# Optimization experiments

Hardware: AMD Instinct MI355X
Metric: run time of the kernel (lower is better)

The kernel has to match this reference:

```python
import jax, jax.numpy as jnp
import numpy as np

N_FEAT = 256
N_HID = 128
N_HEAD = 4
N_HEAD_LAST = 6
N_CLASS = 40
NEG_SLOPE = 0.2


def gat_conv(x, src, dst, W, att_src, att_dst, bias, heads, ch, concat):
    # x: [N, in], W: [in, heads*ch], att_*: [heads, ch]
    N = x.shape[0]
    xw = (x @ W).reshape(N, heads, ch)                      # [N, H, C]
    a_src = jnp.sum(xw * att_src, axis=-1)                  # [N, H]
    a_dst = jnp.sum(xw * att_dst, axis=-1)                  # [N, H]
    e = jax.nn.leaky_relu(a_src[src] + a_dst[dst], NEG_SLOPE)  # [E, H]
    # softmax over incoming edges of each destination node
    m = jax.ops.segment_max(e, dst, num_segments=N)         # [N, H]
    ex = jnp.exp(e - m[dst])
    denom = jax.ops.segment_sum(ex, dst, num_segments=N)    # [N, H]
    alpha = ex / (denom[dst] + 1e-16)                       # [E, H]
    msg = xw[src] * alpha[..., None]                        # [E, H, C]
    out = jax.ops.segment_sum(msg, dst, num_segments=N)     # [N, H, C]
    out = out.reshape(N, heads * ch) if concat else out.mean(axis=1)
    return out + bias


def setup_inputs() -> dict:
    key = jax.random.key(0)
    ks = jax.random.split(key, 16)
    N, E = 10000, 160000
    x = jax.random.normal(ks[0], (N, N_FEAT), dtype=jnp.float32)
    edge_index = jax.random.randint(ks[1], (2, E), 0, N, dtype=jnp.int64)
    hid = N_HID * N_HEAD  # 512
    s = lambda fan: 1.0 / np.sqrt(fan)
    return {
        "x": x,
        "edge_index": edge_index,
        "W0": jax.random.normal(ks[2], (N_FEAT, hid), jnp.float32) * s(N_FEAT),
        "a_src0": jax.random.normal(ks[3], (N_HEAD, N_HID), jnp.float32) * s(N_HID),
        "a_dst0": jax.random.normal(ks[4], (N_HEAD, N_HID), jnp.float32) * s(N_HID),
        "b0": jnp.zeros((hid,), jnp.float32),
        "Wskip_in": jax.random.normal(ks[5], (N_FEAT, hid), jnp.float32) * s(N_FEAT),
        "W1": jax.random.normal(ks[6], (hid, hid), jnp.float32) * s(hid),
        "a_src1": jax.random.normal(ks[7], (N_HEAD, N_HID), jnp.float32) * s(N_HID),
        "a_dst1": jax.random.normal(ks[8], (N_HEAD, N_HID), jnp.float32) * s(N_HID),
        "b1": jnp.zeros((hid,), jnp.float32),
        "W2": jax.random.normal(ks[9], (hid, N_HEAD_LAST * N_CLASS), jnp.float32) * s(hid),
        "a_src2": jax.random.normal(ks[10], (N_HEAD_LAST, N_CLASS), jnp.float32) * s(N_CLASS),
        "a_dst2": jax.random.normal(ks[11], (N_HEAD_LAST, N_CLASS), jnp.float32) * s(N_CLASS),
        "b2": jnp.zeros((N_CLASS,), jnp.float32),
        "Wskip_out": jax.random.normal(ks[12], (hid, N_CLASS), jnp.float32) * s(hid),
    }


def reference(x, edge_index, W0, a_src0, a_dst0, b0, Wskip_in,
              W1, a_src1, a_dst1, b1,
              W2, a_src2, a_dst2, b2, Wskip_out):
    N = x.shape[0]
    loops = jnp.arange(N, dtype=edge_index.dtype)
    src = jnp.concatenate([edge_index[0], loops])  # add self loops (PyG GATConv)
    dst = jnp.concatenate([edge_index[1], loops])
    # eval mode: dropout is identity
    h = gat_conv(x, src, dst, W0, a_src0, a_dst0, b0, N_HEAD, N_HID, True)
    x1 = jax.nn.elu(h + x @ Wskip_in)                      # res skip w/ projection
    h = gat_conv(x1, src, dst, W1, a_src1, a_dst1, b1, N_HEAD, N_HID, True)
    x2 = jax.nn.elu(h + x1)                                # res skip, same dims
    h = gat_conv(x2, src, dst, W2, a_src2, a_dst2, b2, N_HEAD_LAST, N_CLASS, False)
    out = h + x2 @ Wskip_out                               # out_skip 'res'
    return out
```

## Files before the change

kernel.cpp:

```cpp
#include <hip/hip_runtime.h>
#include <math.h>


#define N_FEAT 256
#define HID 512

using u16 = unsigned short;
using bf16x8 = __attribute__((ext_vector_type(8))) __bf16;
using f32x16 = __attribute__((ext_vector_type(16))) float;

__device__ inline u16 bf16_rne(float f) {
    unsigned u = __float_as_uint(f);
    return (u16)((u + 0x7fffu + ((u >> 16) & 1u)) >> 16);
}
__device__ inline float bf16_to_f32(u16 h) {
    return __uint_as_float((unsigned)h << 16);
}
__device__ inline bf16x8 ldb8(const u16* p) {
    return *reinterpret_cast<const bf16x8*>(p);
}


__global__ void init_counts(int* cursor, int N) {
    int i = blockIdx.x * blockDim.x + threadIdx.x;
    if (i < N) cursor[i] = 1;
}

__global__ void count_edges(const int* __restrict__ ei, int E, int* cursor) {
    int e = blockIdx.x * blockDim.x + threadIdx.x;
    if (e < E) atomicAdd(&cursor[ei[E + e]], 1);
}

__global__ __launch_bounds__(1024) void scan_offsets(int* cursor, int* row_off, int N) {
    __shared__ int sdata[1024];
    int tid = threadIdx.x;
    int chunk = (N + 1023) >> 10;
    int base = tid * chunk;
    int lsum = 0;
    for (int i = 0; i < chunk; i++) {
        int idx = base + i;
        if (idx < N) lsum += cursor[idx];
    }
    sdata[tid] = lsum;
    __syncthreads();
    for (int off = 1; off < 1024; off <<= 1) {
        int t = (tid >= off) ? sdata[tid - off] : 0;
        __syncthreads();
        sdata[tid] += t;
        __syncthreads();
    }
    int run = sdata[tid] - lsum;
    if (tid == 0) row_off[0] = 0;
    for (int i = 0; i < chunk; i++) {
        int idx = base + i;
        if (idx < N) {
            int c = cursor[idx];
            cursor[idx] = run;
            run += c;
            row_off[idx + 1] = run;
        }
    }
}

__global__ void fill_csr(const int* __restrict__ ei, int E, int N,
                         int* cursor, int* __restrict__ col) {
    int i = blockIdx.x * blockDim.x + threadIdx.x;
    int tot = E + N;
    if (i >= tot) return;
    int s, d;
    if (i < E) { s = ei[i]; d = ei[E + i]; }
    else       { s = i - E; d = s; }
    int pos = atomicAdd(&cursor[d], 1);
    col[pos] = s;
}


__global__ __launch_bounds__(256) void att_combine(const float* __restrict__ W,
                                                   const float* __restrict__ as_,
                                                   const float* __restrict__ ad_,
                                                   float* __restrict__ ac,
                                                   int K, int H, int C) {
    int i = blockIdx.x * blockDim.x + threadIdx.x;
    if (i >= K * 2 * H) return;
    int k = i / (2 * H);
    int hh = i - k * 2 * H;
    int h = (hh >= H) ? hh - H : hh;
    const float* av = (hh >= H) ? &ad_[h * C] : &as_[h * C];
    const float* wp = &W[(size_t)k * H * C + (size_t)h * C];
    float sum = 0.f;
    for (int c = 0; c < C; c++) sum = fmaf(wp[c], av[c], sum);
    ac[(size_t)k * 2 * H + hh] = sum;
}


__global__ __launch_bounds__(256) void cvtA_pack(const float* __restrict__ X,
                                                 u16* __restrict__ hi, u16* __restrict__ lo,
                                                 int M, int K, int Rblocks) {
    int gid = blockIdx.x * blockDim.x + threadIdx.x;
    int lane = gid & 63;
    int rest = gid >> 6;
    int KC = K >> 4;
    int R = rest / KC;
    int c = rest - R * KC;
    if (R >= Rblocks) return;
    int row = R * 32 + (lane & 31);
    if (row >= M) row = M - 1;
    const float* src = X + (size_t)row * K + c * 16 + (lane >> 5) * 8;
    float4 v0 = *reinterpret_cast<const float4*>(src);
    float4 v1 = *reinterpret_cast<const float4*>(src + 4);
    float vv[8] = {v0.x, v0.y, v0.z, v0.w, v1.x, v1.y, v1.z, v1.w};
    unsigned hp[4], lp[4];
    #pragma unroll
    for (int j = 0; j < 4; j++) {
        u16 h0 = bf16_rne(vv[2 * j]);
        u16 h1 = bf16_rne(vv[2 * j + 1]);
        float r0 = vv[2 * j]     - __uint_as_float((unsigned)h0 << 16);
        float r1 = vv[2 * j + 1] - __uint_as_float((unsigned)h1 << 16);
        u16 l0 = bf16_rne(r0);
        u16 l1 = bf16_rne(r1);
        hp[j] = (unsigned)h0 | ((unsigned)h1 << 16);
        lp[j] = (unsigned)l0 | ((unsigned)l1 << 16);
    }
    size_t dst = ((size_t)rest * 64 + lane) * 8;
    *reinterpret_cast<int4*>(hi + dst) = make_int4(hp[0], hp[1], hp[2], hp[3]);
    *reinterpret_cast<int4*>(lo + dst) = make_int4(lp[0], lp[1], lp[2], lp[3]);
}

__global__ __launch_bounds__(256) void cvtB_pack(const float* __restrict__ B,
                                                 u16* __restrict__ hi, u16* __restrict__ lo,
                                                 int K, int Nb, int Cblocks) {
    int gid = blockIdx.x * blockDim.x + threadIdx.x;
    int lane = gid & 63;
    int rest = gid >> 6;
    int KC = K >> 4;
    int Cb = rest / KC;
    int c = rest - Cb * KC;
    if (Cb >= Cblocks) return;
    int n = Cb * 32 + (lane & 31);
    int kbase = c * 16 + (lane >> 5) * 8;
    float vv[8];
    #pragma unroll
    for (int j = 0; j < 8; j++)
        vv[j] = (n < Nb) ? B[(size_t)(kbase + j) * Nb + n] : 0.f;
    unsigned hp[4], lp[4];
    #pragma unroll
    for (int j = 0; j < 4; j++) {
        u16 h0 = bf16_rne(vv[2 * j]);
        u16 h1 = bf16_rne(vv[2 * j + 1]);
        float r0 = vv[2 * j]     - __uint_as_float((unsigned)h0 << 16);
        float r1 = vv[2 * j + 1] - __uint_as_float((unsigned)h1 << 16);
        u16 l0 = bf16_rne(r0);
        u16 l1 = bf16_rne(r1);
        hp[j] = (unsigned)h0 | ((unsigned)h1 << 16);
        lp[j] = (unsigned)l0 | ((unsigned)l1 << 16);
    }
    size_t dst = ((size_t)rest * 64 + lane) * 8;
    *reinterpret_cast<int4*>(hi + dst) = make_int4(hp[0], hp[1], hp[2], hp[3]);
    *reinterpret_cast<int4*>(lo + dst) = make_int4(lp[0], lp[1], lp[2], lp[3]);
}


__global__ __launch_bounds__(256) void gemm_fused(const u16* __restrict__ Ahi,
                                                  const u16* __restrict__ Alo,
                                                  const u16* __restrict__ Bhi,
                                                  const u16* __restrict__ Blo,
                                                  u16* __restrict__ xwb, int xwCols,
                                                  float* __restrict__ skipP,
                                                  int skipBeg, int skipEnd,
                                                  float* __restrict__ asrc,
                                                  float* __restrict__ adst,
                                                  int attBeg, int H,
                                                  int M, int K,
                                                  int ntiles, int Rblocks) {
    int nwg = gridDim.x, b = blockIdx.x;
    int q = nwg >> 3, r = nwg & 7;
    int xcd = b & 7, idx = b >> 3;
    int t = (xcd < r) ? (xcd * (q + 1) + idx)
                      : (r * (q + 1) + (xcd - r) * q + idx);
    int bm = (t / ntiles) * 128;
    int bn = (t - (t / ntiles) * ntiles) * 64;

    int lane = threadIdx.x & 63, w = threadIdx.x >> 6;
    int wr = w >> 1, wc = w & 1;
    int l31 = lane & 31, lg = lane >> 5;
    int KC = K >> 4;

    int R0 = (bm + wr * 64) >> 5;
    int R1 = R0 + 1;
    if (R0 >= Rblocks) R0 = Rblocks - 1;
    if (R1 >= Rblocks) R1 = Rblocks - 1;
    int Cb = (bn + wc * 32) >> 5;

    const u16* pa0h = Ahi + (((size_t)R0 * KC) * 64 + lane) * 8;
    const u16* pa0l = Alo + (((size_t)R0 * KC) * 64 + lane) * 8;
    const u16* pa1h = Ahi + (((size_t)R1 * KC) * 64 + lane) * 8;
    const u16* pa1l = Alo + (((size_t)R1 * KC) * 64 + lane) * 8;
    const u16* pbh  = Bhi + (((size_t)Cb * KC) * 64 + lane) * 8;
    const u16* pbl  = Blo + (((size_t)Cb * KC) * 64 + lane) * 8;

    f32x16 acc0, acc1;
    #pragma unroll
    for (int i2 = 0; i2 < 16; i2++) { acc0[i2] = 0.f; acc1[i2] = 0.f; }

    bf16x8 a0h = ldb8(pa0h), a0l = ldb8(pa0l);
    bf16x8 a1h = ldb8(pa1h), a1l = ldb8(pa1l);
    bf16x8 bh  = ldb8(pbh),  bl  = ldb8(pbl);

    for (int c = 1; c <= KC; c++) {
        size_t off = (size_t)c * 512;
        bf16x8 na0h = ldb8(pa0h + off), na0l = ldb8(pa0l + off);
        bf16x8 na1h = ldb8(pa1h + off), na1l = ldb8(pa1l + off);
        bf16x8 nbh  = ldb8(pbh + off),  nbl  = ldb8(pbl + off);
        acc0 = __builtin_amdgcn_mfma_f32_32x32x16_bf16(a0h, bh, acc0, 0, 0, 0);
        acc1 = __builtin_amdgcn_mfma_f32_32x32x16_bf16(a1h, bh, acc1, 0, 0, 0);
        acc0 = __builtin_amdgcn_mfma_f32_32x32x16_bf16(a0h, bl, acc0, 0, 0, 0);
        acc1 = __builtin_amdgcn_mfma_f32_32x32x16_bf16(a1h, bl, acc1, 0, 0, 0);
        acc0 = __builtin_amdgcn_mfma_f32_32x32x16_bf16(a0l, bh, acc0, 0, 0, 0);
        acc1 = __builtin_amdgcn_mfma_f32_32x32x16_bf16(a1l, bh, acc1, 0, 0, 0);
        a0h = na0h; a0l = na0l; a1h = na1h; a1l = na1l; bh = nbh; bl = nbl;
    }

    int n = bn + wc * 32 + l31;
    int base_m = bm + wr * 64;
    #pragma unroll
    for (int rg = 0; rg < 16; rg++) {
        int mrow = (rg & 3) + 8 * (rg >> 2) + 4 * lg;
        int m0 = base_m + mrow;
        int m1 = m0 + 32;
        float v0 = acc0[rg], v1 = acc1[rg];
        if (n < xwCols) {
            if (m0 < M) xwb[(size_t)m0 * xwCols + n] = bf16_rne(v0);
            if (m1 < M) xwb[(size_t)m1 * xwCols + n] = bf16_rne(v1);
        } else if (n >= skipBeg && n < skipEnd) {
            int cc = n - skipBeg, st = skipEnd - skipBeg;
            if (m0 < M) skipP[(size_t)m0 * st + cc] = v0;
            if (m1 < M) skipP[(size_t)m1 * st + cc] = v1;
        } else if (n >= attBeg && n < attBeg + H) {
            int h = n - attBeg;
            if (m0 < M) asrc[(size_t)m0 * H + h] = v0;
            if (m1 < M) asrc[(size_t)m1 * H + h] = v1;
        } else if (n >= attBeg + H && n < attBeg + 2 * H) {
            int h = n - attBeg - H;
            if (m0 < M) adst[(size_t)m0 * H + h] = v0;
            if (m1 < M) adst[(size_t)m1 * H + h] = v1;
        }
    }
}


template <int H, int CHUNKS>
__global__ __launch_bounds__(256) void edge_alpha_fused(const float* __restrict__ asrc,
                                                        const float* __restrict__ adst,
                                                        const int* __restrict__ row_off,
                                                        const int* __restrict__ col,
                                                        float* __restrict__ alpha,
                                                        int N) {
    int w = (blockIdx.x * blockDim.x + threadIdx.x) >> 6;
    int lane = threadIdx.x & 63;
    if (w >= N) return;
    int jb = row_off[w], je = row_off[w + 1];

    float adn[H];
    #pragma unroll
    for (int h = 0; h < H; h++) adn[h] = adst[(size_t)w * H + h];

    float ev[CHUNKS][H];
    float m[H];
    #pragma unroll
    for (int h = 0; h < H; h++) m[h] = -INFINITY;

    #pragma unroll
    for (int c = 0; c < CHUNKS; c++) {
        int j = jb + c * 64 + lane;
        if (j < je) {
            int s = col[j];
            const float* ap = &asrc[(size_t)s * H];
            #pragma unroll
            for (int h = 0; h < H; h++) {
                float e = ap[h] + adn[h];
                e = e > 0.f ? e : 0.2f * e;
                ev[c][h] = e;
                m[h] = fmaxf(m[h], e);
            }
        } else {
            #pragma unroll
            for (int h = 0; h < H; h++) ev[c][h] = -INFINITY;
        }
    }
    for (int j = jb + CHUNKS * 64 + lane; j < je; j += 64) {
        int s = col[j];
        const float* ap = &asrc[(size_t)s * H];
        #pragma unroll
        for (int h = 0; h < H; h++) {
            float e = ap[h] + adn[h];
            e = e > 0.f ? e : 0.2f * e;
            m[h] = fmaxf(m[h], e);
        }
    }

    #pragma unroll
    for (int off = 32; off; off >>= 1)
        #pragma unroll
        for (int h = 0; h < H; h++) m[h] = fmaxf(m[h], __shfl_xor(m[h], off));

    float ssum[H];
    #pragma unroll
    for (int h = 0; h < H; h++) ssum[h] = 0.f;
    #pragma unroll
    for (int c = 0; c < CHUNKS; c++)
        #pragma unroll
        for (int h = 0; h < H; h++) ssum[h] += __expf(ev[c][h] - m[h]);
    for (int j = jb + CHUNKS * 64 + lane; j < je; j += 64) {
        int s = col[j];
        const float* ap = &asrc[(size_t)s * H];
        #pragma unroll
        for (int h = 0; h < H; h++) {
            float e = ap[h] + adn[h];
            e = e > 0.f ? e : 0.2f * e;
            ssum[h] += __expf(e - m[h]);
        }
    }
    #pragma unroll
    for (int off = 32; off; off >>= 1)
        #pragma unroll
        for (int h = 0; h < H; h++) ssum[h] += __shfl_xor(ssum[h], off);

    float inv[H];
    #pragma unroll
    for (int h = 0; h < H; h++) inv[h] = 1.f / (ssum[h] + 1e-16f);

    #pragma unroll
    for (int c = 0; c < CHUNKS; c++) {
        int j = jb + c * 64 + lane;
        if (j < je) {
            float* op = &alpha[(size_t)j * H];
            #pragma unroll
            for (int h = 0; h < H; h++)
                op[h] = __expf(ev[c][h] - m[h]) * inv[h];
        }
    }
    for (int j = jb + CHUNKS * 64 + lane; j < je; j += 64) {
        int s = col[j];
        const float* ap = &asrc[(size_t)s * H];
        float* op = &alpha[(size_t)j * H];
        #pragma unroll
        for (int h = 0; h < H; h++) {
            float e = ap[h] + adn[h];
            e = e > 0.f ? e : 0.2f * e;
            op[h] = __expf(e - m[h]) * inv[h];
        }
    }
}


template <int SKIPPK>
__global__ __launch_bounds__(256) void agg_fused512(const u16* __restrict__ xw,
                                                    const float* __restrict__ alpha,
                                                    const int* __restrict__ row_off,
                                                    const int* __restrict__ col,
                                                    const float* __restrict__ bias,
                                                    const float* __restrict__ skipF,
                                                    const u16* __restrict__ skipHi,
                                                    const u16* __restrict__ skipLo,
                                                    u16* __restrict__ outHi,
                                                    u16* __restrict__ outLo,
                                                    int N) {
    int w = (blockIdx.x * blockDim.x + threadIdx.x) >> 6;
    int lane = threadIdx.x & 63;
    if (w >= N) return;
    int base = lane * 8;
    int hme = lane >> 4;

    float acc[8] = {};
    int jb = row_off[w], je = row_off[w + 1];

    int j = jb;
    for (; j + 3 < je; j += 4) {
        int s0 = col[j], s1 = col[j + 1], s2 = col[j + 2], s3 = col[j + 3];
        float a0 = alpha[(size_t)(j + 0) * 4 + hme];
        float a1 = alpha[(size_t)(j + 1) * 4 + hme];
        float a2 = alpha[(size_t)(j + 2) * 4 + hme];
        float a3 = alpha[(size_t)(j + 3) * 4 + hme];
        uint4 r0 = *reinterpret_cast<const uint4*>(&xw[(size_t)s0 * 512 + base]);
        uint4 r1 = *reinterpret_cast<const uint4*>(&xw[(size_t)s1 * 512 + base]);
        uint4 r2 = *reinterpret_cast<const uint4*>(&xw[(size_t)s2 * 512 + base]);
        uint4 r3 = *reinterpret_cast<const uint4*>(&xw[(size_t)s3 * 512 + base]);
        acc[0] = fmaf(a0, __uint_as_float(r0.x << 16), acc[0]);
        acc[1] = fmaf(a0, __uint_as_float(r0.x & 0xffff0000u), acc[1]);
        acc[2] = fmaf(a0, __uint_as_float(r0.y << 16), acc[2]);
        acc[3] = fmaf(a0, __uint_as_float(r0.y & 0xffff0000u), acc[3]);
        acc[4] = fmaf(a0, __uint_as_float(r0.z << 16), acc[4]);
        acc[5] = fmaf(a0, __uint_as_float(r0.z & 0xffff0000u), acc[5]);
        acc[6] = fmaf(a0, __uint_as_float(r0.w << 16), acc[6]);
        acc[7] = fmaf(a0, __uint_as_float(r0.w & 0xffff0000u), acc[7]);
        acc[0] = fmaf(a1, __uint_as_float(r1.x << 16), acc[0]);
        acc[1] = fmaf(a1, __uint_as_float(r1.x & 0xffff0000u), acc[1]);
        acc[2] = fmaf(a1, __uint_as_float(r1.y << 16), acc[2]);
        acc[3] = fmaf(a1, __uint_as_float(r1.y & 0xffff0000u), acc[3]);
        acc[4] = fmaf(a1, __uint_as_float(r1.z << 16), acc[4]);
        acc[5] = fmaf(a1, __uint_as_float(r1.z & 0xffff0000u), acc[5]);
        acc[6] = fmaf(a1, __uint_as_float(r1.w << 16), acc[6]);
        acc[7] = fmaf(a1, __uint_as_float(r1.w & 0xffff0000u), acc[7]);
        acc[0] = fmaf(a2, __uint_as_float(r2.x << 16), acc[0]);
        acc[1] = fmaf(a2, __uint_as_float(r2.x & 0xffff0000u), acc[1]);
        acc[2] = fmaf(a2, __uint_as_float(r2.y << 16), acc[2]);
        acc[3] = fmaf(a2, __uint_as_float(r2.y & 0xffff0000u), acc[3]);
        acc[4] = fmaf(a2, __uint_as_float(r2.z << 16), acc[4]);
        acc[5] = fmaf(a2, __uint_as_float(r2.z & 0xffff0000u), acc[5]);
        acc[6] = fmaf(a2, __uint_as_float(r2.w << 16), acc[6]);
        acc[7] = fmaf(a2, __uint_as_float(r2.w & 0xffff0000u), acc[7]);
        acc[0] = fmaf(a3, __uint_as_float(r3.x << 16), acc[0]);
        acc[1] = fmaf(a3, __uint_as_float(r3.x & 0xffff0000u), acc[1]);
        acc[2] = fmaf(a3, __uint_as_float(r3.y << 16), acc[2]);
        acc[3] = fmaf(a3, __uint_as_float(r3.y & 0xffff0000u), acc[3]);
        acc[4] = fmaf(a3, __uint_as_float(r3.z << 16), acc[4]);
        acc[5] = fmaf(a3, __uint_as_float(r3.z & 0xffff0000u), acc[5]);
        acc[6] = fmaf(a3, __uint_as_float(r3.w << 16), acc[6]);
        acc[7] = fmaf(a3, __uint_as_float(r3.w & 0xffff0000u), acc[7]);
    }
    for (; j < je; ++j) {
        int s = col[j];
        float a = alpha[(size_t)j * 4 + hme];
        uint4 raw = *reinterpret_cast<const uint4*>(&xw[(size_t)s * 512 + base]);
        acc[0] = fmaf(a, __uint_as_float(raw.x << 16), acc[0]);
        acc[1] = fmaf(a, __uint_as_float(raw.x & 0xffff0000u), acc[1]);
        acc[2] = fmaf(a, __uint_as_float(raw.y << 16), acc[2]);
        acc[3] = fmaf(a, __uint_as_float(raw.y & 0xffff0000u), acc[3]);
        acc[4] = fmaf(a, __uint_as_float(raw.z << 16), acc[4]);
        acc[5] = fmaf(a, __uint_as_float(raw.z & 0xffff0000u), acc[5]);
        acc[6] = fmaf(a, __uint_as_float(raw.w << 16), acc[6]);
        acc[7] = fmaf(a, __uint_as_float(raw.w & 0xffff0000u), acc[7]);
    }

    int R = w >> 5, r31 = w & 31, cc = lane >> 1, sub = lane & 1;
    int lp = r31 | (sub << 5);
    size_t slot = (((size_t)R * 32 + cc) * 64 + lp) * 8;

    float sk[8];
    if (SKIPPK) {
        int4 h4 = *reinterpret_cast<const int4*>(skipHi + slot);
        int4 l4 = *reinterpret_cast<const int4*>(skipLo + slot);
        unsigned hu[4] = {(unsigned)h4.x, (unsigned)h4.y, (unsigned)h4.z, (unsigned)h4.w};
        unsigned lu[4] = {(unsigned)l4.x, (unsigned)l4.y, (unsigned)l4.z, (unsigned)l4.w};
        #pragma unroll
        for (int i = 0; i < 4; i++) {
            sk[2 * i]     = __uint_as_float(hu[i] << 16) + __uint_as_float(lu[i] << 16);
            sk[2 * i + 1] = __uint_as_float(hu[i] & 0xffff0000u)
                          + __uint_as_float(lu[i] & 0xffff0000u);
        }
    } else {
        const float* kp = &skipF[(size_t)w * 512 + base];
        float4 s0 = *reinterpret_cast<const float4*>(kp);
        float4 s1 = *reinterpret_cast<const float4*>(kp + 4);
        sk[0] = s0.x; sk[1] = s0.y; sk[2] = s0.z; sk[3] = s0.w;
        sk[4] = s1.x; sk[5] = s1.y; sk[6] = s1.z; sk[7] = s1.w;
    }

    const float* bp = &bias[base];
    float r[8];
    #pragma unroll
    for (int i = 0; i < 8; i++) {
        float v = acc[i] + bp[i] + sk[i];
        r[i] = v > 0.f ? v : expm1f(v);
    }

    unsigned hp[4], lpk[4];
    #pragma unroll
    for (int i = 0; i < 4; i++) {
        u16 h0 = bf16_rne(r[2 * i]);
        u16 h1 = bf16_rne(r[2 * i + 1]);
        float q0 = r[2 * i]     - __uint_as_float((unsigned)h0 << 16);
        float q1 = r[2 * i + 1] - __uint_as_float((unsigned)h1 << 16);
        u16 l0 = bf16_rne(q0);
        u16 l1 = bf16_rne(q1);
        hp[i]  = (unsigned)h0 | ((unsigned)h1 << 16);
        lpk[i] = (unsigned)l0 | ((unsigned)l1 << 16);
    }
    *reinterpret_cast<int4*>(outHi + slot) = make_int4(hp[0], hp[1], hp[2], hp[3]);
    *reinterpret_cast<int4*>(outLo + slot) = make_int4(lpk[0], lpk[1], lpk[2], lpk[3]);
}


__global__ __launch_bounds__(256) void agg_final240(const u16* __restrict__ xw,
                                                    const float* __restrict__ alpha,
                                                    const int* __restrict__ row_off,
                                                    const int* __restrict__ col,
                                                    const float* __restrict__ b2,
                                                    const float* __restrict__ skip,
                                                    float* __restrict__ out,
                                                    int N) {
    int w = (blockIdx.x * blockDim.x + threadIdx.x) >> 6;
    int lane = threadIdx.x & 63;
    if (w >= N) return;
    bool active = lane < 40;

    float acc[6] = {};
    int jb = row_off[w], je = row_off[w + 1];

    int j = jb;
    for (; j + 1 < je; j += 2) {
        int s0 = col[j], s1 = col[j + 1];
        const float* ap0 = &alpha[(size_t)j * 6];
        const float* ap1 = &alpha[(size_t)(j + 1) * 6];
        if (active) {
            const u16* sp0 = &xw[(size_t)s0 * 240 + lane];
            const u16* sp1 = &xw[(size_t)s1 * 240 + lane];
            #pragma unroll
            for (int h = 0; h < 6; h++) {
                acc[h] = fmaf(ap0[h], bf16_to_f32(sp0[h * 40]), acc[h]);
                acc[h] = fmaf(ap1[h], bf16_to_f32(sp1[h * 40]), acc[h]);
            }
        }
    }
    for (; j < je; ++j) {
        int s = col[j];
        const float* ap = &alpha[(size_t)j * 6];
        if (active) {
            const u16* sp = &xw[(size_t)s * 240 + lane];
            #pragma unroll
            for (int h = 0; h < 6; h++)
                acc[h] = fmaf(ap[h], bf16_to_f32(sp[h * 40]), acc[h]);
        }
    }
    if (active) {
        float v = (acc[0] + acc[1] + acc[2] + acc[3] + acc[4] + acc[5]) * (1.f / 6.f)
                  + b2[lane] + skip[(size_t)w * 40 + lane];
        out[(size_t)w * 40 + lane] = v;
    }
}


extern "C" void kernel_launch(void* const* d_in, const int* in_sizes, int n_in,
                              void* d_out, int out_size, void* d_ws, size_t ws_size,
                              hipStream_t stream) {
    const float* x        = (const float*)d_in[0];
    const int*   ei       = (const int*)  d_in[1];
    const float* W0       = (const float*)d_in[2];
    const float* a_src0   = (const float*)d_in[3];
    const float* a_dst0   = (const float*)d_in[4];
    const float* b0       = (const float*)d_in[5];
    const float* Wskip_in = (const float*)d_in[6];
    const float* W1       = (const float*)d_in[7];
    const float* a_src1   = (const float*)d_in[8];
    const float* a_dst1   = (const float*)d_in[9];
    const float* b1       = (const float*)d_in[10];
    const float* W2       = (const float*)d_in[11];
    const float* a_src2   = (const float*)d_in[12];
    const float* a_dst2   = (const float*)d_in[13];
    const float* b2       = (const float*)d_in[14];
    const float* Wskip_out= (const float*)d_in[15];

    const int N = in_sizes[0] / N_FEAT;
    const int E = in_sizes[1] / 2;
    float* out = (float*)d_out;

    const int Rblocks = (N + 31) / 32;
    const int mtiles = (N + 127) / 128;

    float* ws = (float*)d_ws;
    size_t o = 0;
    u16* xwb   = (u16*)(ws + o); o += (size_t)N * 256;
    float* tmpD  = ws + o; o += (size_t)N * HID;
    float* asrc  = ws + o; o += (size_t)N * 8;
    float* adst  = ws + o; o += (size_t)N * 8;
    float* skipo = ws + o; o += (size_t)N * 40;
    float* alpha = ws + o; o += (size_t)(E + N) * 6;
    float* ac    = ws + o; o += (size_t)512 * 12;

    u16* up = (u16*)(ws + o);
    size_t uo = 0;
    const size_t aPack = (size_t)Rblocks * 32 * 512 + 512;
    u16* AhA = up + uo; uo += aPack;   u16* AlA = up + uo; uo += aPack;
    u16* AhB = up + uo; uo += aPack;   u16* AlB = up + uo; uo += aPack;
    const size_t b0sz = (size_t)34 * 16 * 512 + 512;
    u16* B0h = up + uo; uo += b0sz;  u16* B0l = up + uo; uo += b0sz;
    const size_t b1sz = (size_t)18 * 32 * 512 + 512;
    u16* B1h = up + uo; uo += b1sz;  u16* B1l = up + uo; uo += b1sz;
    const size_t b2sz = (size_t)12 * 32 * 512 + 512;
    u16* B2h = up + uo; uo += b2sz;  u16* B2l = up + uo; uo += b2sz;
    int* row_off = (int*)(up + uo);
    int* cursor  = row_off + (N + 1);
    int* col     = cursor + (N + 1);

    init_counts<<<(N + 255) / 256, 256, 0, stream>>>(cursor, N);
    count_edges<<<(E + 255) / 256, 256, 0, stream>>>(ei, E, cursor);
    scan_offsets<<<1, 1024, 0, stream>>>(cursor, row_off, N);
    fill_csr<<<(E + N + 255) / 256, 256, 0, stream>>>(ei, E, N, cursor, col);

    cvtB_pack<<<(16 * 16 * 64 + 255) / 256, 256, 0, stream>>>(W0, B0h, B0l, 256, 512, 16);
    cvtB_pack<<<(16 * 16 * 64 + 255) / 256, 256, 0, stream>>>(
        Wskip_in, B0h + (size_t)16 * 16 * 512, B0l + (size_t)16 * 16 * 512, 256, 512, 16);
    att_combine<<<(256 * 8 + 255) / 256, 256, 0, stream>>>(W0, a_src0, a_dst0, ac, 256, 4, 128);
    cvtB_pack<<<(2 * 16 * 64 + 255) / 256, 256, 0, stream>>>(
        ac, B0h + (size_t)32 * 16 * 512, B0l + (size_t)32 * 16 * 512, 256, 8, 2);
    cvtB_pack<<<(16 * 32 * 64 + 255) / 256, 256, 0, stream>>>(W1, B1h, B1l, 512, 512, 16);
    att_combine<<<(512 * 8 + 255) / 256, 256, 0, stream>>>(W1, a_src1, a_dst1, ac, 512, 4, 128);
    cvtB_pack<<<(2 * 32 * 64 + 255) / 256, 256, 0, stream>>>(
        ac, B1h + (size_t)16 * 32 * 512, B1l + (size_t)16 * 32 * 512, 512, 8, 2);
    cvtB_pack<<<(8 * 32 * 64 + 255) / 256, 256, 0, stream>>>(W2, B2h, B2l, 512, 240, 8);
    cvtB_pack<<<(2 * 32 * 64 + 255) / 256, 256, 0, stream>>>(
        Wskip_out, B2h + (size_t)8 * 32 * 512, B2l + (size_t)8 * 32 * 512, 512, 40, 2);
    att_combine<<<(512 * 12 + 255) / 256, 256, 0, stream>>>(W2, a_src2, a_dst2, ac, 512, 6, 40);
    cvtB_pack<<<(2 * 32 * 64 + 255) / 256, 256, 0, stream>>>(
        ac, B2h + (size_t)10 * 32 * 512, B2l + (size_t)10 * 32 * 512, 512, 12, 2);

    int nodeBlocks = (N * 64 + 255) / 256;
    const int BIG = 1 << 30;

    cvtA_pack<<<(Rblocks * 16 * 64 + 255) / 256, 256, 0, stream>>>(x, AhA, AlA, N, 256, Rblocks);
    gemm_fused<<<mtiles * 17, 256, 0, stream>>>(
        AhA, AlA, B0h, B0l, xwb, 512, tmpD, 512, 1024, asrc, adst, 1024, 4,
        N, 256, 17, Rblocks);
    edge_alpha_fused<4, 4><<<nodeBlocks, 256, 0, stream>>>(asrc, adst, row_off, col, alpha, N);
    agg_fused512<0><<<nodeBlocks, 256, 0, stream>>>(
        xwb, alpha, row_off, col, b0, tmpD, nullptr, nullptr, AhB, AlB, N);

    gemm_fused<<<mtiles * 9, 256, 0, stream>>>(
        AhB, AlB, B1h, B1l, xwb, 512, nullptr, BIG, BIG, asrc, adst, 512, 4,
        N, 512, 9, Rblocks);
    edge_alpha_fused<4, 4><<<nodeBlocks, 256, 0, stream>>>(asrc, adst, row_off, col, alpha, N);
    agg_fused512<1><<<nodeBlocks, 256, 0, stream>>>(
        xwb, alpha, row_off, col, b1, nullptr, AhB, AlB, AhA, AlA, N);

    gemm_fused<<<mtiles * 6, 256, 0, stream>>>(
        AhA, AlA, B2h, B2l, xwb, 240, skipo, 256, 296, asrc, adst, 320, 6,
        N, 512, 6, Rblocks);
    edge_alpha_fused<6, 4><<<nodeBlocks, 256, 0, stream>>>(asrc, adst, row_off, col, alpha, N);
    agg_final240<<<nodeBlocks, 256, 0, stream>>>(
        xwb, alpha, row_off, col, b2, skipo, out, N);
}
```

Measured before the change: 415.6 us.

## Fuse edge softmax into aggregation via shared memory and batch weight packing launches

The separate per-layer edge_alpha kernel is folded into the aggregation kernels. Each wave computes its node's attention softmax, keeps the source indices and alpha values in LDS, and then gathers from LDS, so the global alpha array write and re-read go away. Nodes with more than 256 edges recompute alpha on the fly for the overflow edges. Separately, the many small att_combine and cvtB_pack launches are merged into two launches. This adds LDS use (about 20KB per block) and a block barrier, which may lower occupancy.

```diff
diff --git a/kernel.cpp b/kernel.cpp
--- a/kernel.cpp
+++ b/kernel.cpp
@@ -75,18 +75,24 @@
 }
 
 
-__global__ __launch_bounds__(256) void att_combine(const float* __restrict__ W,
-                                                   const float* __restrict__ as_,
-                                                   const float* __restrict__ ad_,
-                                                   float* __restrict__ ac,
-                                                   int K, int H, int C) {
+__global__ __launch_bounds__(256) void att_combine_all(
+        const float* __restrict__ W0, const float* __restrict__ as0, const float* __restrict__ ad0,
+        const float* __restrict__ W1, const float* __restrict__ as1, const float* __restrict__ ad1,
+        const float* __restrict__ W2, const float* __restrict__ as2, const float* __restrict__ ad2,
+        float* __restrict__ ac0, float* __restrict__ ac1, float* __restrict__ ac2) {
     int i = blockIdx.x * blockDim.x + threadIdx.x;
-    if (i >= K * 2 * H) return;
-    int k = i / (2 * H);
-    int hh = i - k * 2 * H;
+    const float *W, *as_, *ad_;
+    float* ac;
+    int K, H, C, li;
+    if (i < 2048)       { W = W0; as_ = as0; ad_ = ad0; ac = ac0; K = 256; H = 4; C = 128; li = i; }
+    else if (i < 6144)  { W = W1; as_ = as1; ad_ = ad1; ac = ac1; K = 512; H = 4; C = 128; li = i - 2048; }
+    else if (i < 12288) { W = W2; as_ = as2; ad_ = ad2; ac = ac2; K = 512; H = 6; C = 40;  li = i - 6144; }
+    else return;
+    int k = li / (2 * H);
+    int hh = li - k * 2 * H;
     int h = (hh >= H) ? hh - H : hh;
-    const float* av = (hh >= H) ? &ad_[h * C] : &as_[h * C];
-    const float* wp = &W[(size_t)k * H * C + (size_t)h * C];
+    const float* av = ((hh >= H) ? ad_ : as_) + h * C;
+    const float* wp = W + (size_t)k * H * C + (size_t)h * C;
     float sum = 0.f;
     for (int c = 0; c < C; c++) sum = fmaf(wp[c], av[c], sum);
     ac[(size_t)k * 2 * H + hh] = sum;
@@ -126,16 +132,14 @@
     *reinterpret_cast<int4*>(lo + dst) = make_int4(lp[0], lp[1], lp[2], lp[3]);
 }
 
-__global__ __launch_bounds__(256) void cvtB_pack(const float* __restrict__ B,
-                                                 u16* __restrict__ hi, u16* __restrict__ lo,
-                                                 int K, int Nb, int Cblocks) {
-    int gid = blockIdx.x * blockDim.x + threadIdx.x;
+__device__ inline void cvtB_body(const float* __restrict__ B,
+                                 u16* __restrict__ hi, u16* __restrict__ lo,
+                                 int K, int Nb, int gid) {
     int lane = gid & 63;
     int rest = gid >> 6;
     int KC = K >> 4;
     int Cb = rest / KC;
     int c = rest - Cb * KC;
-    if (Cb >= Cblocks) return;
     int n = Cb * 32 + (lane & 31);
     int kbase = c * 16 + (lane >> 5) * 8;
     float vv[8];
@@ -157,6 +161,24 @@
     size_t dst = ((size_t)rest * 64 + lane) * 8;
     *reinterpret_cast<int4*>(hi + dst) = make_int4(hp[0], hp[1], hp[2], hp[3]);
     *reinterpret_cast<int4*>(lo + dst) = make_int4(lp[0], lp[1], lp[2], lp[3]);
+}
+
+__global__ __launch_bounds__(256) void pack_all_B(
+        const float* __restrict__ W0, const float* __restrict__ Wsi, const float* __restrict__ ac0,
+        const float* __restrict__ W1, const float* __restrict__ ac1,
+        const float* __restrict__ W2, const float* __restrict__ Wso, const float* __restrict__ ac2,
+        u16* __restrict__ B0h, u16* __restrict__ B0l,
+        u16* __restrict__ B1h, u16* __restrict__ B1l,
+        u16* __restrict__ B2h, u16* __restrict__ B2l) {
+    int g = blockIdx.x * blockDim.x + threadIdx.x;
+    if (g < 16384)      cvtB_body(W0,  B0h, B0l, 256, 512, g);
+    else if (g < 32768) cvtB_body(Wsi, B0h + (size_t)16 * 16 * 512, B0l + (size_t)16 * 16 * 512, 256, 512, g - 16384);
+    else if (g < 34816) cvtB_body(ac0, B0h + (size_t)32 * 16 * 512, B0l + (size_t)32 * 16 * 512, 256, 8,   g - 32768);
+    else if (g < 67584) cvtB_body(W1,  B1h, B1l, 512, 512, g - 34816);
+    else if (g < 71680) cvtB_body(ac1, B1h + (size_t)16 * 32 * 512, B1l + (size_t)16 * 32 * 512, 512, 8,   g - 67584);
+    else if (g < 88064) cvtB_body(W2,  B2h, B2l, 512, 240, g - 71680);
+    else if (g < 92160) cvtB_body(Wso, B2h + (size_t)8 * 32 * 512,  B2l + (size_t)8 * 32 * 512,  512, 40,  g - 88064);
+    else if (g < 96256) cvtB_body(ac2, B2h + (size_t)10 * 32 * 512, B2l + (size_t)10 * 32 * 512, 512, 12,  g - 92160);
 }
 
 
@@ -248,143 +270,125 @@
 }
 
 
-template <int H, int CHUNKS>
-__global__ __launch_bounds__(256) void edge_alpha_fused(const float* __restrict__ asrc,
-                                                        const float* __restrict__ adst,
-                                                        const int* __restrict__ row_off,
-                                                        const int* __restrict__ col,
-                                                        float* __restrict__ alpha,
-                                                        int N) {
+template <int SKIPPK>
+__global__ __launch_bounds__(256) void agg_sm512(const u16* __restrict__ xw,
+                                                 const float* __restrict__ asrc,
+                                                 const float* __restrict__ adst,
+                                                 const int* __restrict__ row_off,
+                                                 const int* __restrict__ col,
+                                                 const float* __restrict__ bias,
+                                                 const float* __restrict__ skipF,
+                                                 const u16* __restrict__ skipHi,
+                                                 const u16* __restrict__ skipLo,
+                                                 u16* __restrict__ outHi,
+                                                 u16* __restrict__ outLo,
+                                                 int N) {
+    __shared__ float lalpha[4][256 * 4];
+    __shared__ int   lcol[4][256];
     int w = (blockIdx.x * blockDim.x + threadIdx.x) >> 6;
     int lane = threadIdx.x & 63;
-    if (w >= N) return;
-    int jb = row_off[w], je = row_off[w + 1];
-
-    float adn[H];
-    #pragma unroll
-    for (int h = 0; h < H; h++) adn[h] = adst[(size_t)w * H + h];
-
-    float ev[CHUNKS][H];
-    float m[H];
-    #pragma unroll
-    for (int h = 0; h < H; h++) m[h] = -INFINITY;
-
-    #pragma unroll
-    for (int c = 0; c < CHUNKS; c++) {
-        int j = jb + c * 64 + lane;
-        if (j < je) {
+    int wid = (threadIdx.x >> 6) & 3;
+    bool valid = w < N;
+    int jb = 0, je = 0;
+    float adn[4], m[4], inv[4];
+
+    if (valid) {
+        jb = row_off[w]; je = row_off[w + 1];
+        float4 ad4 = *reinterpret_cast<const float4*>(&adst[(size_t)w * 4]);
+        adn[0] = ad4.x; adn[1] = ad4.y; adn[2] = ad4.z; adn[3] = ad4.w;
+
+        float ev[4][4];
+        int scol[4];
+        #pragma unroll
+        for (int h = 0; h < 4; h++) m[h] = -INFINITY;
+
+        #pragma unroll
+        for (int c = 0; c < 4; c++) {
+            int j = jb + c * 64 + lane;
+            if (j < je) {
+                int s = col[j]; scol[c] = s;
+                float4 as4 = *reinterpret_cast<const float4*>(&asrc[(size_t)s * 4]);
+                float e0 = as4.x + adn[0]; e0 = e0 > 0.f ? e0 : 0.2f * e0;
+                float e1 = as4.y + adn[1]; e1 = e1 > 0.f ? e1 : 0.2f * e1;
+                float e2 = as4.z + adn[2]; e2 = e2 > 0.f ? e2 : 0.2f * e2;
+                float e3 = as4.w + adn[3]; e3 = e3 > 0.f ? e3 : 0.2f * e3;
+                ev[c][0] = e0; ev[c][1] = e1; ev[c][2] = e2; ev[c][3] = e3;
+                m[0] = fmaxf(m[0], e0); m[1] = fmaxf(m[1], e1);
+                m[2] = fmaxf(m[2], e2); m[3] = fmaxf(m[3], e3);
+            } else {
+                scol[c] = -1;
+                #pragma unroll
+                for (int h = 0; h < 4; h++) ev[c][h] = -INFINITY;
+            }
+        }
+        for (int j = jb + 256 + lane; j < je; j += 64) {
             int s = col[j];
-            const float* ap = &asrc[(size_t)s * H];
-            #pragma unroll
-            for (int h = 0; h < H; h++) {
-                float e = ap[h] + adn[h];
+            #pragma unroll
+            for (int h = 0; h < 4; h++) {
+                float e = asrc[(size_t)s * 4 + h] + adn[h];
                 e = e > 0.f ? e : 0.2f * e;
-                ev[c][h] = e;
                 m[h] = fmaxf(m[h], e);
             }
-        } else {
-            #pragma unroll
-            for (int h = 0; h < H; h++) ev[c][h] = -INFINITY;
-        }
-    }
-    for (int j = jb + CHUNKS * 64 + lane; j < je; j += 64) {
-        int s = col[j];
-        const float* ap = &asrc[(size_t)s * H];
-        #pragma unroll
-        for (int h = 0; h < H; h++) {
-            float e = ap[h] + adn[h];
-            e = e > 0.f ? e : 0.2f * e;
-            m[h] = fmaxf(m[h], e);
-        }
-    }
-
-    #pragma unroll
-    for (int off = 32; off; off >>= 1)
-        #pragma unroll
-        for (int h = 0; h < H; h++) m[h] = fmaxf(m[h], __shfl_xor(m[h], off));
-
-    float ssum[H];
-    #pragma unroll
-    for (int h = 0; h < H; h++) ssum[h] = 0.f;
-    #pragma unroll
-    for (int c = 0; c < CHUNKS; c++)
-        #pragma unroll
-        for (int h = 0; h < H; h++) ssum[h] += __expf(ev[c][h] - m[h]);
-    for (int j = jb + CHUNKS * 64 + lane; j < je; j += 64) {
-        int s = col[j];
-        const float* ap = &asrc[(size_t)s * H];
-        #pragma unroll
-        for (int h = 0; h < H; h++) {
-            float e = ap[h] + adn[h];
-            e = e > 0.f ? e : 0.2f * e;
-            ssum[h] += __expf(e - m[h]);
-        }
-    }
-    #pragma unroll
-    for (int off = 32; off; off >>= 1)
-        #pragma unroll
-        for (int h = 0; h < H; h++) ssum[h] += __shfl_xor(ssum[h], off);
-
-    float inv[H];
-    #pragma unroll
-    for (int h = 0; h < H; h++) inv[h] = 1.f / (ssum[h] + 1e-16f);
-
-    #pragma unroll
-    for (int c = 0; c < CHUNKS; c++) {
-        int j = jb + c * 64 + lane;
-        if (j < je) {
-            float* op = &alpha[(size_t)j * H];
-            #pragma unroll
-            for (int h = 0; h < H; h++)
-                op[h] = __expf(ev[c][h] - m[h]) * inv[h];
-        }
-    }
-    for (int j = jb + CHUNKS * 64 + lane; j < je; j += 64) {
-        int s = col[j];
-        const float* ap = &asrc[(size_t)s * H];
-        float* op = &alpha[(size_t)j * H];
-        #pragma unroll
-        for (int h = 0; h < H; h++) {
-            float e = ap[h] + adn[h];
-            e = e > 0.f ? e : 0.2f * e;
-            op[h] = __expf(e - m[h]) * inv[h];
-        }
-    }
-}
-
-
-template <int SKIPPK>
-__global__ __launch_bounds__(256) void agg_fused512(const u16* __restrict__ xw,
-                                                    const float* __restrict__ alpha,
-                                                    const int* __restrict__ row_off,
-                                                    const int* __restrict__ col,
-                                                    const float* __restrict__ bias,
-                                                    const float* __restrict__ skipF,
-                                                    const u16* __restrict__ skipHi,
-                                                    const u16* __restrict__ skipLo,
-                                                    u16* __restrict__ outHi,
-                                                    u16* __restrict__ outLo,
-                                                    int N) {
-    int w = (blockIdx.x * blockDim.x + threadIdx.x) >> 6;
-    int lane = threadIdx.x & 63;
-    if (w >= N) return;
+        }
+        #pragma unroll
+        for (int off = 32; off; off >>= 1)
+            #pragma unroll
+            for (int h = 0; h < 4; h++) m[h] = fmaxf(m[h], __shfl_xor(m[h], off));
+
+        float ssum[4] = {0.f, 0.f, 0.f, 0.f};
+        #pragma unroll
+        for (int c = 0; c < 4; c++)
+            #pragma unroll
+            for (int h = 0; h < 4; h++) ssum[h] += __expf(ev[c][h] - m[h]);
+        for (int j = jb + 256 + lane; j < je; j += 64) {
+            int s = col[j];
+            #pragma unroll
+            for (int h = 0; h < 4; h++) {
+                float e = asrc[(size_t)s * 4 + h] + adn[h];
+                e = e > 0.f ? e : 0.2f * e;
+                ssum[h] += __expf(e - m[h]);
+            }
+        }
+        #pragma unroll
+        for (int off = 32; off; off >>= 1)
+            #pragma unroll
+            for (int h = 0; h < 4; h++) ssum[h] += __shfl_xor(ssum[h], off);
+        #pragma unroll
+        for (int h = 0; h < 4; h++) inv[h] = 1.f / (ssum[h] + 1e-16f);
+
+        #pragma unroll
+        for (int c = 0; c < 4; c++) {
+            int rel = c * 64 + lane;
+            if (jb + rel < je) {
+                lcol[wid][rel] = scol[c];
+                *reinterpret_cast<float4*>(&lalpha[wid][rel * 4]) = make_float4(
+                    __expf(ev[c][0] - m[0]) * inv[0],
+                    __expf(ev[c][1] - m[1]) * inv[1],
+                    __expf(ev[c][2] - m[2]) * inv[2],
+                    __expf(ev[c][3] - m[3]) * inv[3]);
+            }
+        }
+    }
+    __syncthreads();
+    if (!valid) return;
+
     int base = lane * 8;
     int hme = lane >> 4;
-
     float acc[8] = {};
-    int jb = row_off[w], je = row_off[w + 1];
-
-    int j = jb;
-    for (; j + 3 < je; j += 4) {
-        int s0 = col[j], s1 = col[j + 1], s2 = col[j + 2], s3 = col[j + 3];
-        float a0 = alpha[(size_t)(j + 0) * 4 + hme];
-        float a1 = alpha[(size_t)(j + 1) * 4 + hme];
-        float a2 = alpha[(size_t)(j + 2) * 4 + hme];
-        float a3 = alpha[(size_t)(j + 3) * 4 + hme];
-        uint4 r0 = *reinterpret_cast<const uint4*>(&xw[(size_t)s0 * 512 + base]);
-        uint4 r1 = *reinterpret_cast<const uint4*>(&xw[(size_t)s1 * 512 + base]);
-        uint4 r2 = *reinterpret_cast<const uint4*>(&xw[(size_t)s2 * 512 + base]);
-        uint4 r3 = *reinterpret_cast<const uint4*>(&xw[(size_t)s3 * 512 + base]);
+    int deg = je - jb;
+    int fast = deg < 256 ? deg : 256;
+
+    int j = 0;
+    for (; j + 3 < fast; j += 4) {
+        int4 cs = *reinterpret_cast<const int4*>(&lcol[wid][j]);
+        float a0 = lalpha[wid][(j + 0) * 4 + hme];
+        float a1 = lalpha[wid][(j + 1) * 4 + hme];
+        float a2 = lalpha[wid][(j + 2) * 4 + hme];
+        float a3 = lalpha[wid][(j + 3) * 4 + hme];
+        uint4 r0 = *reinterpret_cast<const uint4*>(&xw[(size_t)cs.x * 512 + base]);
+        uint4 r1 = *reinterpret_cast<const uint4*>(&xw[(size_t)cs.y * 512 + base]);
+        uint4 r2 = *reinterpret_cast<const uint4*>(&xw[(size_t)cs.z * 512 + base]);
+        uint4 r3 = *reinterpret_cast<const uint4*>(&xw[(size_t)cs.w * 512 + base]);
         acc[0] = fmaf(a0, __uint_as_float(r0.x << 16), acc[0]);
         acc[1] = fmaf(a0, __uint_as_float(r0.x & 0xffff0000u), acc[1]);
         acc[2] = fmaf(a0, __uint_as_float(r0.y << 16), acc[2]);
@@ -418,9 +422,9 @@
         acc[6] = fmaf(a3, __uint_as_float(r3.w << 16), acc[6]);
         acc[7] = fmaf(a3, __uint_as_float(r3.w & 0xffff0000u), acc[7]);
     }
-    for (; j < je; ++j) {
-        int s = col[j];
-        float a = alpha[(size_t)j * 4 + hme];
+    for (; j < fast; ++j) {
+        int s = lcol[wid][j];
+        float a = lalpha[wid][j * 4 + hme];
         uint4 raw = *reinterpret_cast<const uint4*>(&xw[(size_t)s * 512 + base]);
         acc[0] = fmaf(a, __uint_as_float(raw.x << 16), acc[0]);
         acc[1] = fmaf(a, __uint_as_float(raw.x & 0xffff0000u), acc[1]);
@@ -430,6 +434,26 @@
         acc[5] = fmaf(a, __uint_as_float(raw.z & 0xffff0000u), acc[5]);
         acc[6] = fmaf(a, __uint_as_float(raw.w << 16), acc[6]);
         acc[7] = fmaf(a, __uint_as_float(raw.w & 0xffff0000u), acc[7]);
+    }
+    if (deg > 256) {
+        float adn_h = hme == 0 ? adn[0] : hme == 1 ? adn[1] : hme == 2 ? adn[2] : adn[3];
+        float m_h   = hme == 0 ? m[0]   : hme == 1 ? m[1]   : hme == 2 ? m[2]   : m[3];
+        float inv_h = hme == 0 ? inv[0] : hme == 1 ? inv[1] : hme == 2 ? inv[2] : inv[3];
+        for (int jj = jb + 256; jj < je; ++jj) {
+            int s = col[jj];
+            float e = asrc[(size_t)s * 4 + hme] + adn_h;
+            e = e > 0.f ? e : 0.2f * e;
+            float a = __expf(e - m_h) * inv_h;
+            uint4 raw = *reinterpret_cast<const uint4*>(&xw[(size_t)s * 512 + base]);
+            acc[0] = fmaf(a, __uint_as_float(raw.x << 16), acc[0]);
+            acc[1] = fmaf(a, __uint_as_float(raw.x & 0xffff0000u), acc[1]);
+            acc[2] = fmaf(a, __uint_as_float(raw.y << 16), acc[2]);
+            acc[3] = fmaf(a, __uint_as_float(raw.y & 0xffff0000u), acc[3]);
+            acc[4] = fmaf(a, __uint_as_float(raw.z << 16), acc[4]);
+            acc[5] = fmaf(a, __uint_as_float(raw.z & 0xffff0000u), acc[5]);
+            acc[6] = fmaf(a, __uint_as_float(raw.w << 16), acc[6]);
+            acc[7] = fmaf(a, __uint_as_float(raw.w & 0xffff0000u), acc[7]);
+        }
     }
 
     int R = w >> 5, r31 = w & 31, cc = lane >> 1, sub = lane & 1;
@@ -481,27 +505,111 @@
 }
 
 
-__global__ __launch_bounds__(256) void agg_final240(const u16* __restrict__ xw,
-                                                    const float* __restrict__ alpha,
-                                                    const int* __restrict__ row_off,
-                                                    const int* __restrict__ col,
-                                                    const float* __restrict__ b2,
-                                                    const float* __restrict__ skip,
-                                                    float* __restrict__ out,
-                                                    int N) {
+__global__ __launch_bounds__(256) void agg_final240_sm(const u16* __restrict__ xw,
+                                                       const float* __restrict__ asrc,
+                                                       const float* __restrict__ adst,
+                                                       const int* __restrict__ row_off,
+                                                       const int* __restrict__ col,
+                                                       const float* __restrict__ b2,
+                                                       const float* __restrict__ skip,
+                                                       float* __restrict__ out,
+                                                       int N) {
+    __shared__ float lalpha[4][256 * 6];
+    __shared__ int   lcol[4][256];
     int w = (blockIdx.x * blockDim.x + threadIdx.x) >> 6;
     int lane = threadIdx.x & 63;
-    if (w >= N) return;
+    int wid = (threadIdx.x >> 6) & 3;
+    bool valid = w < N;
+    int jb = 0, je = 0;
+    float adn[6], m[6], inv[6];
+
+    if (valid) {
+        jb = row_off[w]; je = row_off[w + 1];
+        #pragma unroll
+        for (int h = 0; h < 6; h++) adn[h] = adst[(size_t)w * 6 + h];
+
+        float ev[4][6];
+        int scol[4];
+        #pragma unroll
+        for (int h = 0; h < 6; h++) m[h] = -INFINITY;
+
+        #pragma unroll
+        for (int c = 0; c < 4; c++) {
+            int j = jb + c * 64 + lane;
+            if (j < je) {
+                int s = col[j]; scol[c] = s;
+                #pragma unroll
+                for (int h = 0; h < 6; h++) {
+                    float e = asrc[(size_t)s * 6 + h] + adn[h];
+                    e = e > 0.f ? e : 0.2f * e;
+                    ev[c][h] = e;
+                    m[h] = fmaxf(m[h], e);
+                }
+            } else {
+                scol[c] = -1;
+                #pragma unroll
+                for (int h = 0; h < 6; h++) ev[c][h] = -INFINITY;
+            }
+        }
+        for (int j = jb + 256 + lane; j < je; j += 64) {
+            int s = col[j];
+            #pragma unroll
+            for (int h = 0; h < 6; h++) {
+                float e = asrc[(size_t)s * 6 + h] + adn[h];
+                e = e > 0.f ? e : 0.2f * e;
+                m[h] = fmaxf(m[h], e);
+            }
+        }
+        #pragma unroll
+        for (int off = 32; off; off >>= 1)
+            #pragma unroll
+            for (int h = 0; h < 6; h++) m[h] = fmaxf(m[h], __shfl_xor(m[h], off));
+
+        float ssum[6] = {0.f, 0.f, 0.f, 0.f, 0.f, 0.f};
+        #pragma unroll
+        for (int c = 0; c < 4; c++)
+            #pragma unroll
+            for (int h = 0; h < 6; h++) ssum[h] += __expf(ev[c][h] - m[h]);
+        for (int j = jb + 256 + lane; j < je; j += 64) {
+            int s = col[j];
+            #pragma unroll
+            for (int h = 0; h < 6; h++) {
+                float e = asrc[(size_t)s * 6 + h] + adn[h];
+                e = e > 0.f ? e : 0.2f * e;
+                ssum[h] += __expf(e - m[h]);
+            }
+        }
+        #pragma unroll
+        for (int off = 32; off; off >>= 1)
+            #pragma unroll
+            for (int h = 0; h < 6; h++) ssum[h] += __shfl_xor(ssum[h], off);
+        #pragma unroll
+        for (int h = 0; h < 6; h++) inv[h] = 1.f / (ssum[h] + 1e-16f);
+
+        #pragma unroll
+        for (int c = 0; c < 4; c++) {
+            int rel = c * 64 + lane;
+            if (jb + rel < je) {
+                lcol[wid][rel] = scol[c];
+                #pragma unroll
+                for (int h = 0; h < 6; h++)
+                    lalpha[wid][rel * 6 + h] = __expf(ev[c][h] - m[h]) * inv[h];
+            }
+        }
+    }
+    __syncthreads();
+    if (!valid) return;
+
     bool active = lane < 40;
-
     float acc[6] = {};
-    int jb = row_off[w], je = row_off[w + 1];
-
-    int j = jb;
-    for (; j + 1 < je; j += 2) {
-        int s0 = col[j], s1 = col[j + 1];
-        const float* ap0 = &alpha[(size_t)j * 6];
-        const float* ap1 = &alpha[(size_t)(j + 1) * 6];
+    int deg = je - jb;
+    int fast = deg < 256 ? deg : 256;
+
+    int j = 0;
+    for (; j + 1 < fast; j += 2) {
+        int s0 = lcol[wid][j], s1 = lcol[wid][j + 1];
+        const float* ap0 = &lalpha[wid][j * 6];
+        const float* ap1 = &lalpha[wid][(j + 1) * 6];
         if (active) {
             const u16* sp0 = &xw[(size_t)s0 * 240 + lane];
             const u16* sp1 = &xw[(size_t)s1 * 240 + lane];
@@ -512,14 +620,29 @@
             }
         }
     }
-    for (; j < je; ++j) {
-        int s = col[j];
-        const float* ap = &alpha[(size_t)j * 6];
+    for (; j < fast; ++j) {
+        int s = lcol[wid][j];
+        const float* ap = &lalpha[wid][j * 6];
         if (active) {
             const u16* sp = &xw[(size_t)s * 240 + lane];
             #pragma unroll
             for (int h = 0; h < 6; h++)
                 acc[h] = fmaf(ap[h], bf16_to_f32(sp[h * 40]), acc[h]);
+        }
+    }
+    if (deg > 256) {
+        for (int jj = jb + 256; jj < je; ++jj) {
+            int s = col[jj];
+            if (active) {
+                const u16* sp = &xw[(size_t)s * 240 + lane];
+                #pragma unroll
+                for (int h = 0; h < 6; h++) {
+                    float e = asrc[(size_t)s * 6 + h] + adn[h];
+                    e = e > 0.f ? e : 0.2f * e;
+                    float a = __expf(e - m[h]) * inv[h];
+                    acc[h] = fmaf(a, bf16_to_f32(sp[h * 40]), acc[h]);
+                }
+            }
         }
     }
     if (active) {
@@ -564,8 +687,9 @@
     float* asrc  = ws + o; o += (size_t)N * 8;
     float* adst  = ws + o; o += (size_t)N * 8;
     float* skipo = ws + o; o += (size_t)N * 40;
-    float* alpha = ws + o; o += (size_t)(E + N) * 6;
-    float* ac    = ws + o; o += (size_t)512 * 12;
+    float* ac0   = ws + o; o += 256 * 8;
+    float* ac1   = ws + o; o += 512 * 8;
+    float* ac2   = ws + o; o += 512 * 12;
 
     u16* up = (u16*)(ws + o);
     size_t uo = 0;
@@ -587,22 +711,12 @@
     scan_offsets<<<1, 1024, 0, stream>>>(cursor, row_off, N);
     fill_csr<<<(E + N + 255) / 256, 256, 0, stream>>>(ei, E, N, cursor, col);
 
-    cvtB_pack<<<(16 * 16 * 64 + 255) / 256, 256, 0, stream>>>(W0, B0h, B0l, 256, 512, 16);
-    cvtB_pack<<<(16 * 16 * 64 + 255) / 256, 256, 0, stream>>>(
-        Wskip_in, B0h + (size_t)16 * 16 * 512, B0l + (size_t)16 * 16 * 512, 256, 512, 16);
-    att_combine<<<(256 * 8 + 255) / 256, 256, 0, stream>>>(W0, a_src0, a_dst0, ac, 256, 4, 128);
-    cvtB_pack<<<(2 * 16 * 64 + 255) / 256, 256, 0, stream>>>(
-        ac, B0h + (size_t)32 * 16 * 512, B0l + (size_t)32 * 16 * 512, 256, 8, 2);
-    cvtB_pack<<<(16 * 32 * 64 + 255) / 256, 256, 0, stream>>>(W1, B1h, B1l, 512, 512, 16);
-    att_combine<<<(512 * 8 + 255) / 256, 256, 0, stream>>>(W1, a_src1, a_dst1, ac, 512, 4, 128);
-    cvtB_pack<<<(2 * 32 * 64 + 255) / 256, 256, 0, stream>>>(
-        ac, B1h + (size_t)16 * 32 * 512, B1l + (size_t)16 * 32 * 512, 512, 8, 2);
-    cvtB_pack<<<(8 * 32 * 64 + 255) / 256, 256, 0, stream>>>(W2, B2h, B2l, 512, 240, 8);
-    cvtB_pack<<<(2 * 32 * 64 + 255) / 256, 256, 0, stream>>>(
-        Wskip_out, B2h + (size_t)8 * 32 * 512, B2l + (size_t)8 * 32 * 512, 512, 40, 2);
-    att_combine<<<(512 * 12 + 255) / 256, 256, 0, stream>>>(W2, a_src2, a_dst2, ac, 512, 6, 40);
-    cvtB_pack<<<(2 * 32 * 64 + 255) / 256, 256, 0, stream>>>(
-        ac, B2h + (size_t)10 * 32 * 512, B2l + (size_t)10 * 32 * 512, 512, 12, 2);
+    att_combine_all<<<48, 256, 0, stream>>>(W0, a_src0, a_dst0,
+                                            W1, a_src1, a_dst1,
+                                            W2, a_src2, a_dst2, ac0, ac1, ac2);
+    pack_all_B<<<376, 256, 0, stream>>>(W0, Wskip_in, ac0, W1, ac1,
+                                        W2, Wskip_out, ac2,
+                                        B0h, B0l, B1h, B1l, B2h, B2l);
 
     int nodeBlocks = (N * 64 + 255) / 256;
     const int BIG = 1 << 30;
@@ -611,21 +725,18 @@
     gemm_fused<<<mtiles * 17, 256, 0, stream>>>(
         AhA, AlA, B0h, B0l, xwb, 512, tmpD, 512, 1024, asrc, adst, 1024, 4,
         N, 256, 17, Rblocks);
-    edge_alpha_fused<4, 4><<<nodeBlocks, 256, 0, stream>>>(asrc, adst, row_off, col, alpha, N);
-    agg_fused512<0><<<nodeBlocks, 256, 0, stream>>>(
-        xwb, alpha, row_off, col, b0, tmpD, nullptr, nullptr, AhB, AlB, N);
+    agg_sm512<0><<<nodeBlocks, 256, 0, stream>>>(
+        xwb, asrc, adst, row_off, col, b0, tmpD, nullptr, nullptr, AhB, AlB, N);
 
     gemm_fused<<<mtiles * 9, 256, 0, stream>>>(
         AhB, AlB, B1h, B1l, xwb, 512, nullptr, BIG, BIG, asrc, adst, 512, 4,
         N, 512, 9, Rblocks);
-    edge_alpha_fused<4, 4><<<nodeBlocks, 256, 0, stream>>>(asrc, adst, row_off, col, alpha, N);
-    agg_fused512<1><<<nodeBlocks, 256, 0, stream>>>(
-        xwb, alpha, row_off, col, b1, nullptr, AhB, AlB, AhA, AlA, N);
+    agg_sm512<1><<<nodeBlocks, 256, 0, stream>>>(
+        xwb, asrc, adst, row_off, col, b1, nullptr, AhB, AlB, AhA, AlA, N);
 
     gemm_fused<<<mtiles * 6, 256, 0, stream>>>(
         AhA, AlA, B2h, B2l, xwb, 240, skipo, 256, 296, asrc, adst, 320, 6,
         N, 512, 6, Rblocks);
-    edge_alpha_fused<6, 4><<<nodeBlocks, 256, 0, stream>>>(asrc, adst, row_off, col, alpha, N);
-    agg_final240<<<nodeBlocks, 256, 0, stream>>>(
-        xwb, alpha, row_off, col, b2, skipo, out, N);
-}
+    agg_final240_sm<<<nodeBlocks, 256, 0, stream>>>(
+        xwb, asrc, adst, row_off, col, b2, skipo, out, N);
+}
```

New measurement: 343.4 us. 1.21x faster.
